# Kernel optimization log

Hardware: AMD Instinct MI355X
Metric: run time of the kernel (lower is better)

## Reference

```python
import jax, jax.numpy as jnp
import numpy as np

INPUT_DIM = 64
RESERVOIR_DIM = 2048
OUTPUT_DIM = 64
SPECTRAL_RADIUS = 0.9
LEAK_RATE = 0.3
SPARSITY = 0.9
INPUT_SCALING = 1.0
NOISE_LEVEL = 0.01
T = 4096


def setup_inputs() -> dict:
    key = jax.random.key(0)
    k_u, k_n = jax.random.split(key)
    u = jax.random.normal(k_u, (T, INPUT_DIM), dtype=jnp.float32)
    noise = jax.random.normal(k_n, (T, RESERVOIR_DIM), dtype=jnp.float32)

    # Reservoir weights, built exactly like the torch __init__ (fixed, untrained).
    rng = np.random.default_rng(0)
    W_in = (rng.standard_normal((RESERVOIR_DIM, INPUT_DIM)) * INPUT_SCALING).astype(np.float32)
    W = (rng.uniform(0.0, 1.0, (RESERVOIR_DIM, RESERVOIR_DIM)) * 2.0 - 1.0).astype(np.float32)
    mask = rng.uniform(0.0, 1.0, (RESERVOIR_DIM, RESERVOIR_DIM)) > SPARSITY
    W = W * mask.astype(np.float32)
    sr = np.max(np.abs(np.linalg.eigvals(W)))  # spectral radius normalization
    W = (W * (SPECTRAL_RADIUS / sr)).astype(np.float32)

    # nn.Linear(reservoir_dim, output_dim) init: U(-1/sqrt(N), 1/sqrt(N))
    bound = 1.0 / np.sqrt(RESERVOIR_DIM)
    readout_w = rng.uniform(-bound, bound, (OUTPUT_DIM, RESERVOIR_DIM)).astype(np.float32)
    readout_b = rng.uniform(-bound, bound, (OUTPUT_DIM,)).astype(np.float32)

    return {
        "u": u,
        "noise": noise,
        "W_in": jnp.asarray(W_in),
        "W": jnp.asarray(W),
        "readout_w": jnp.asarray(readout_w),
        "readout_b": jnp.asarray(readout_b),
    }


def reference(u, noise, W_in, W, readout_w, readout_b):
    # Leaky-integrated ESN recurrence, state reset to zeros (reset_state=True).
    input_terms = u @ W_in.T + noise * NOISE_LEVEL  # [T, N], precompute input GEMM

    def step(state, it):
        new_state = jnp.tanh(it + W @ state)
        state = (1.0 - LEAK_RATE) * state + LEAK_RATE * new_state
        return state, state

    init = jnp.zeros((RESERVOIR_DIM,), dtype=u.dtype)
    _, states = jax.lax.scan(step, init, input_terms)  # states: [T, N]
    return states @ readout_w.T + readout_b  # [T, output_dim]
```

## Files before the change

### kernel.cpp

```cpp
#include <hip/hip_runtime.h>

#define T_STEPS 4096
#define N_RES   2048
#define N_IN    64
#define N_OUT   64
#define LEAK    0.3f
#define NOISE_S 0.01f

#define NWG      128
#define RPW      16
#define RPWAVE   4
#define NTHREADS 320

typedef unsigned int uint32x4 __attribute__((ext_vector_type(4)));

__global__ __launch_bounds__(256) void input_terms_kernel(
    const float* __restrict__ u, const float* __restrict__ noise,
    const float* __restrict__ W_in, float* __restrict__ it) {
  const int t = blockIdx.x;
  const int tid = threadIdx.x;
  __shared__ float su[N_IN];
  if (tid < N_IN) su[tid] = u[(size_t)t * N_IN + tid];
  __syncthreads();
  #pragma unroll
  for (int k = 0; k < N_RES / 256; ++k) {
    const int n = tid + 256 * k;
    const float4* wr = reinterpret_cast<const float4*>(W_in + (size_t)n * N_IN);
    float acc = 0.f;
    #pragma unroll
    for (int j = 0; j < N_IN / 4; ++j) {
      float4 w4 = wr[j];
      acc = fmaf(w4.x, su[4 * j + 0], acc);
      acc = fmaf(w4.y, su[4 * j + 1], acc);
      acc = fmaf(w4.z, su[4 * j + 2], acc);
      acc = fmaf(w4.w, su[4 * j + 3], acc);
    }
    it[(size_t)t * N_RES + n] = acc + NOISE_S * noise[(size_t)t * N_RES + n];
  }
}

__global__ __launch_bounds__(NTHREADS, 1) void reservoir_kernel(
    const float* __restrict__ W, float* __restrict__ it,
    unsigned int* sbuf) {
  const int wg = blockIdx.x;
  const int tid = threadIdx.x;
  const int wave = tid >> 6;
  const int lane = tid & 63;
  const int R = wg * RPW;

  __shared__ float Wl[RPW * N_RES];
  __shared__ float ls[2][N_RES];

  {
    const float4* Wg = reinterpret_cast<const float4*>(W + (size_t)R * N_RES);
    float4* Wd = reinterpret_cast<float4*>(Wl);
    for (int idx = tid; idx < RPW * N_RES / 4; idx += NTHREADS)
      Wd[idx] = Wg[idx];
  }
  for (int idx = tid; idx < N_RES; idx += NTHREADS) ls[0][idx] = 0.f;
  __syncthreads();

  if (wave < 4) {
    const int r0 = R + wave * RPWAVE;
    const float4* W0 = reinterpret_cast<const float4*>(Wl + (size_t)(RPWAVE * wave + 0) * N_RES);
    const float4* W1 = reinterpret_cast<const float4*>(Wl + (size_t)(RPWAVE * wave + 1) * N_RES);
    const float4* W2 = reinterpret_cast<const float4*>(Wl + (size_t)(RPWAVE * wave + 2) * N_RES);
    const float4* W3 = reinterpret_cast<const float4*>(Wl + (size_t)(RPWAVE * wave + 3) * N_RES);

    float itv = 0.f;
    if (lane < RPWAVE) itv = it[r0 + lane];

    for (unsigned int t = 0; t < T_STEPS; ++t) {
      const float* cur = ls[t & 1];
      float* nxt = ls[(t + 1) & 1];
      unsigned int* swb = sbuf + ((t + 1) & 1) * N_RES;

      const float4* S4 = reinterpret_cast<const float4*>(cur);
      float a0 = 0.f, a1 = 0.f, a2 = 0.f, a3 = 0.f;
      #pragma unroll
      for (int j = 0; j < N_RES / 4 / 64; ++j) {
        const float4 s4 = S4[lane + 64 * j];
        const float4 x0 = W0[lane + 64 * j];
        const float4 x1 = W1[lane + 64 * j];
        const float4 x2 = W2[lane + 64 * j];
        const float4 x3 = W3[lane + 64 * j];
        a0 = fmaf(x0.x, s4.x, a0); a0 = fmaf(x0.y, s4.y, a0);
        a0 = fmaf(x0.z, s4.z, a0); a0 = fmaf(x0.w, s4.w, a0);
        a1 = fmaf(x1.x, s4.x, a1); a1 = fmaf(x1.y, s4.y, a1);
        a1 = fmaf(x1.z, s4.z, a1); a1 = fmaf(x1.w, s4.w, a1);
        a2 = fmaf(x2.x, s4.x, a2); a2 = fmaf(x2.y, s4.y, a2);
        a2 = fmaf(x2.z, s4.z, a2); a2 = fmaf(x2.w, s4.w, a2);
        a3 = fmaf(x3.x, s4.x, a3); a3 = fmaf(x3.y, s4.y, a3);
        a3 = fmaf(x3.z, s4.z, a3); a3 = fmaf(x3.w, s4.w, a3);
      }
      #pragma unroll
      for (int off = 32; off > 0; off >>= 1) {
        a0 += __shfl_xor(a0, off);
        a1 += __shfl_xor(a1, off);
        a2 += __shfl_xor(a2, off);
        a3 += __shfl_xor(a3, off);
      }

      const unsigned int tg = (t + 1) & 3u;
      unsigned int pkw = 0;
      if (lane < RPWAVE) {
        const float a = (lane == 0) ? a0 : (lane == 1) ? a1 : (lane == 2) ? a2 : a3;
        const float h = tanhf(itv + a);
        const float sold = cur[r0 + lane];
        const float snew = (1.0f - LEAK) * sold + LEAK * h;
        pkw = (__float_as_uint(snew) & ~3u) | tg;
        nxt[r0 + lane] = __uint_as_float(pkw);
        it[(size_t)t * N_RES + r0 + lane] = snew;
      }
      uint32x4 pk;
      pk[0] = __shfl(pkw, 0);
      pk[1] = __shfl(pkw, 1);
      pk[2] = __shfl(pkw, 2);
      pk[3] = __shfl(pkw, 3);
      if (lane == 0) {
        uint32x4* dst = reinterpret_cast<uint32x4*>(swb) + (r0 >> 2);
        asm volatile("global_store_dwordx4 %0, %1, off sc0 sc1"
                     :: "v"(dst), "v"(pk) : "memory");
      }
      if (lane < RPWAVE && t + 1 < T_STEPS)
        itv = it[(size_t)(t + 1) * N_RES + r0 + lane];

      __syncthreads();
    }
  } else {
    unsigned int ownmask = 0;
    {
      const int j = lane - ((wg * 4) & 63);
      if (0 <= j && j < 4) ownmask = 1u << (wg >> 4);
    }
    for (unsigned int t = 0; t < T_STEPS; ++t) {
      if (t + 1 < T_STEPS) {
        unsigned int* swb = sbuf + ((t + 1) & 1) * N_RES;
        float* nxt = ls[(t + 1) & 1];
        const unsigned int tg = (t + 1) & 3u;
        const char* p0 = (const char*)swb + lane * 16;
        const char* p1 = p0 + 4096;
        uint32x4* dst = reinterpret_cast<uint32x4*>(nxt);
        unsigned int need = 0xFFu & ~ownmask;
        for (;;) {
          uint32x4 v0, v1, v2, v3, v4, v5, v6, v7;
          asm volatile(
              "global_load_dwordx4 %0, %8, off sc0 sc1\n\t"
              "global_load_dwordx4 %1, %8, off offset:1024 sc0 sc1\n\t"
              "global_load_dwordx4 %2, %8, off offset:2048 sc0 sc1\n\t"
              "global_load_dwordx4 %3, %8, off offset:3072 sc0 sc1\n\t"
              "global_load_dwordx4 %4, %9, off sc0 sc1\n\t"
              "global_load_dwordx4 %5, %9, off offset:1024 sc0 sc1\n\t"
              "global_load_dwordx4 %6, %9, off offset:2048 sc0 sc1\n\t"
              "global_load_dwordx4 %7, %9, off offset:3072 sc0 sc1\n\t"
              "s_waitcnt vmcnt(0)"
              : "=&v"(v0), "=&v"(v1), "=&v"(v2), "=&v"(v3),
                "=&v"(v4), "=&v"(v5), "=&v"(v6), "=&v"(v7)
              : "v"(p0), "v"(p1)
              : "memory");
          if ((need & 1u)   && ((((v0[0]^tg)|(v0[1]^tg)|(v0[2]^tg)|(v0[3]^tg))&3u)==0u)) { dst[lane +   0] = v0; need &= ~1u; }
          if ((need & 2u)   && ((((v1[0]^tg)|(v1[1]^tg)|(v1[2]^tg)|(v1[3]^tg))&3u)==0u)) { dst[lane +  64] = v1; need &= ~2u; }
          if ((need & 4u)   && ((((v2[0]^tg)|(v2[1]^tg)|(v2[2]^tg)|(v2[3]^tg))&3u)==0u)) { dst[lane + 128] = v2; need &= ~4u; }
          if ((need & 8u)   && ((((v3[0]^tg)|(v3[1]^tg)|(v3[2]^tg)|(v3[3]^tg))&3u)==0u)) { dst[lane + 192] = v3; need &= ~8u; }
          if ((need & 16u)  && ((((v4[0]^tg)|(v4[1]^tg)|(v4[2]^tg)|(v4[3]^tg))&3u)==0u)) { dst[lane + 256] = v4; need &= ~16u; }
          if ((need & 32u)  && ((((v5[0]^tg)|(v5[1]^tg)|(v5[2]^tg)|(v5[3]^tg))&3u)==0u)) { dst[lane + 320] = v5; need &= ~32u; }
          if ((need & 64u)  && ((((v6[0]^tg)|(v6[1]^tg)|(v6[2]^tg)|(v6[3]^tg))&3u)==0u)) { dst[lane + 384] = v6; need &= ~64u; }
          if ((need & 128u) && ((((v7[0]^tg)|(v7[1]^tg)|(v7[2]^tg)|(v7[3]^tg))&3u)==0u)) { dst[lane + 448] = v7; need &= ~128u; }
          if (__all(need == 0u)) break;
          __builtin_amdgcn_s_sleep(1);
        }
      }
      __syncthreads();
    }
  }
}

__global__ __launch_bounds__(256) void readout_kernel(
    const float* __restrict__ states, const float* __restrict__ rw,
    const float* __restrict__ rb, float* __restrict__ out) {
  const int t = blockIdx.x;
  const int tid = threadIdx.x;
  const int o = tid & 63;
  const int q = tid >> 6;
  __shared__ float ss[N_RES];
  #pragma unroll
  for (int k = 0; k < N_RES / 256; ++k)
    ss[tid + 256 * k] = states[(size_t)t * N_RES + tid + 256 * k];
  __syncthreads();

  const float4* r4 = reinterpret_cast<const float4*>(rw + (size_t)o * N_RES + q * 512);
  float acc = 0.f;
  #pragma unroll 8
  for (int j = 0; j < 128; ++j) {
    float4 w4 = r4[j];
    const int base = q * 512 + 4 * j;
    acc = fmaf(w4.x, ss[base + 0], acc);
    acc = fmaf(w4.y, ss[base + 1], acc);
    acc = fmaf(w4.z, ss[base + 2], acc);
    acc = fmaf(w4.w, ss[base + 3], acc);
  }
  __shared__ float red[256];
  red[tid] = acc;
  __syncthreads();
  if (tid < 64) {
    float v = red[tid] + red[tid + 64] + red[tid + 128] + red[tid + 192];
    out[(size_t)t * N_OUT + tid] = v + rb[tid];
  }
}

extern "C" void kernel_launch(void* const* d_in, const int* in_sizes, int n_in,
                              void* d_out, int out_size, void* d_ws, size_t ws_size,
                              hipStream_t stream) {
  const float* u     = (const float*)d_in[0];
  const float* noise = (const float*)d_in[1];
  const float* W_in  = (const float*)d_in[2];
  const float* W     = (const float*)d_in[3];
  const float* rw    = (const float*)d_in[4];
  const float* rb    = (const float*)d_in[5];
  float* out = (float*)d_out;

  float* it = (float*)d_ws;
  unsigned int* sbuf =
      (unsigned int*)((char*)d_ws + (size_t)T_STEPS * N_RES * sizeof(float));

  hipMemsetAsync(sbuf, 0, 2 * N_RES * sizeof(unsigned int), stream);

  input_terms_kernel<<<T_STEPS, 256, 0, stream>>>(u, noise, W_in, it);

  void* args[] = {(void*)&W, (void*)&it, (void*)&sbuf};
  hipLaunchCooperativeKernel((void*)reservoir_kernel, dim3(NWG), dim3(NTHREADS),
                             args, 0, stream);

  readout_kernel<<<T_STEPS, 256, 0, stream>>>(it, rw, rb, out);
}
```

Before: 13.11 ms.

## Keep W rows in registers and offload input-term I/O to a helper wave

Each compute wave now loads its four W rows straight into 32 float4 registers instead of staging them in LDS, which removes per-step LDS reads of weights. A sixth wave is added that prefetches the next step's input terms into a small LDS staging buffer and writes finished states back to global memory, taking those global accesses off the compute waves' critical path. This raises register pressure and adds a one-step lag on the state writeback, and the stored states now carry the two low tag bits.

```diff
diff --git a/kernel.cpp b/kernel.cpp
--- a/kernel.cpp
+++ b/kernel.cpp
@@ -10,9 +10,10 @@
 #define NWG      128
 #define RPW      16
 #define RPWAVE   4
-#define NTHREADS 320
+#define NTHREADS 384
 
 typedef unsigned int uint32x4 __attribute__((ext_vector_type(4)));
+typedef float        floatx4 __attribute__((ext_vector_type(4)));
 
 __global__ __launch_bounds__(256) void input_terms_kernel(
     const float* __restrict__ u, const float* __restrict__ noise,
@@ -48,42 +49,54 @@
   const int lane = tid & 63;
   const int R = wg * RPW;
 
-  __shared__ float Wl[RPW * N_RES];
   __shared__ float ls[2][N_RES];
-
-  {
-    const float4* Wg = reinterpret_cast<const float4*>(W + (size_t)R * N_RES);
-    float4* Wd = reinterpret_cast<float4*>(Wl);
-    for (int idx = tid; idx < RPW * N_RES / 4; idx += NTHREADS)
-      Wd[idx] = Wg[idx];
-  }
+  __shared__ float stg_it[2][RPW];
+
   for (int idx = tid; idx < N_RES; idx += NTHREADS) ls[0][idx] = 0.f;
-  __syncthreads();
+  if (wave == 5 && lane < RPW) stg_it[0][lane] = it[R + lane];
 
   if (wave < 4) {
     const int r0 = R + wave * RPWAVE;
-    const float4* W0 = reinterpret_cast<const float4*>(Wl + (size_t)(RPWAVE * wave + 0) * N_RES);
-    const float4* W1 = reinterpret_cast<const float4*>(Wl + (size_t)(RPWAVE * wave + 1) * N_RES);
-    const float4* W2 = reinterpret_cast<const float4*>(Wl + (size_t)(RPWAVE * wave + 2) * N_RES);
-    const float4* W3 = reinterpret_cast<const float4*>(Wl + (size_t)(RPWAVE * wave + 3) * N_RES);
-
-    float itv = 0.f;
-    if (lane < RPWAVE) itv = it[r0 + lane];
+
+    floatx4 w[32];
+    #pragma unroll
+    for (int r = 0; r < RPWAVE; ++r) {
+      const char* p0 = (const char*)(W + (size_t)(r0 + r) * N_RES) + lane * 16;
+      const char* p1 = p0 + 4096;
+      asm volatile(
+          "global_load_dwordx4 %0, %8, off\n\t"
+          "global_load_dwordx4 %1, %8, off offset:1024\n\t"
+          "global_load_dwordx4 %2, %8, off offset:2048\n\t"
+          "global_load_dwordx4 %3, %8, off offset:3072\n\t"
+          "global_load_dwordx4 %4, %9, off\n\t"
+          "global_load_dwordx4 %5, %9, off offset:1024\n\t"
+          "global_load_dwordx4 %6, %9, off offset:2048\n\t"
+          "global_load_dwordx4 %7, %9, off offset:3072"
+          : "=&v"(w[8 * r + 0]), "=&v"(w[8 * r + 1]),
+            "=&v"(w[8 * r + 2]), "=&v"(w[8 * r + 3]),
+            "=&v"(w[8 * r + 4]), "=&v"(w[8 * r + 5]),
+            "=&v"(w[8 * r + 6]), "=&v"(w[8 * r + 7])
+          : "v"(p0), "v"(p1)
+          : "memory");
+    }
+    asm volatile("s_waitcnt vmcnt(0)" ::: "memory");
+    __builtin_amdgcn_sched_barrier(0);
+    __syncthreads();
 
     for (unsigned int t = 0; t < T_STEPS; ++t) {
       const float* cur = ls[t & 1];
       float* nxt = ls[(t + 1) & 1];
       unsigned int* swb = sbuf + ((t + 1) & 1) * N_RES;
 
-      const float4* S4 = reinterpret_cast<const float4*>(cur);
+      const floatx4* S4 = reinterpret_cast<const floatx4*>(cur);
       float a0 = 0.f, a1 = 0.f, a2 = 0.f, a3 = 0.f;
       #pragma unroll
-      for (int j = 0; j < N_RES / 4 / 64; ++j) {
-        const float4 s4 = S4[lane + 64 * j];
-        const float4 x0 = W0[lane + 64 * j];
-        const float4 x1 = W1[lane + 64 * j];
-        const float4 x2 = W2[lane + 64 * j];
-        const float4 x3 = W3[lane + 64 * j];
+      for (int j = 0; j < 8; ++j) {
+        const floatx4 s4 = S4[lane + 64 * j];
+        const floatx4 x0 = w[j];
+        const floatx4 x1 = w[8 + j];
+        const floatx4 x2 = w[16 + j];
+        const floatx4 x3 = w[24 + j];
         a0 = fmaf(x0.x, s4.x, a0); a0 = fmaf(x0.y, s4.y, a0);
         a0 = fmaf(x0.z, s4.z, a0); a0 = fmaf(x0.w, s4.w, a0);
         a1 = fmaf(x1.x, s4.x, a1); a1 = fmaf(x1.y, s4.y, a1);
@@ -105,12 +118,12 @@
       unsigned int pkw = 0;
       if (lane < RPWAVE) {
         const float a = (lane == 0) ? a0 : (lane == 1) ? a1 : (lane == 2) ? a2 : a3;
+        const float itv = stg_it[t & 1][wave * RPWAVE + lane];
         const float h = tanhf(itv + a);
         const float sold = cur[r0 + lane];
         const float snew = (1.0f - LEAK) * sold + LEAK * h;
         pkw = (__float_as_uint(snew) & ~3u) | tg;
         nxt[r0 + lane] = __uint_as_float(pkw);
-        it[(size_t)t * N_RES + r0 + lane] = snew;
       }
       uint32x4 pk;
       pk[0] = __shfl(pkw, 0);
@@ -122,12 +135,10 @@
         asm volatile("global_store_dwordx4 %0, %1, off sc0 sc1"
                      :: "v"(dst), "v"(pk) : "memory");
       }
-      if (lane < RPWAVE && t + 1 < T_STEPS)
-        itv = it[(size_t)(t + 1) * N_RES + r0 + lane];
-
       __syncthreads();
     }
-  } else {
+  } else if (wave == 4) {
+    __syncthreads();
     unsigned int ownmask = 0;
     {
       const int j = lane - ((wg * 4) & 63);
@@ -172,6 +183,19 @@
       }
       __syncthreads();
     }
+  } else {
+    __syncthreads();
+    for (unsigned int t = 0; t < T_STEPS; ++t) {
+      if (lane < RPW) {
+        if (t >= 1)
+          it[(size_t)(t - 1) * N_RES + R + lane] = ls[t & 1][R + lane];
+        if (t + 1 < T_STEPS)
+          stg_it[(t + 1) & 1][lane] = it[(size_t)(t + 1) * N_RES + R + lane];
+      }
+      __syncthreads();
+    }
+    if (lane < RPW)
+      it[(size_t)(T_STEPS - 1) * N_RES + R + lane] = ls[T_STEPS & 1][R + lane];
   }
 }
 
```

New measurement: 14.23 ms. 8.5% more time.

## Spread reservoir rows over 256 workgroups and offload input and state I/O to a dedicated wave

Applied to the files above, without the earlier changes.

Halves the rows per workgroup, from 16 to 8, and doubles the workgroup count to 256, so each compute wave does a 2-row dot product per step instead of 4. The per-row flag granularity in the shared exchange buffer becomes 8-byte halves, with matching dwordx2 publish stores and poll checks. A new seventh wave prefetches the next step's input term into LDS and writes the previous state back to global memory, taking that latency off the compute waves. In exchange, twice as many workgroups must meet at the cross-workgroup barrier each step. The two poller waves also duplicate the same polling work, and the stored states carry the 2-bit tag in their low mantissa bits.

```diff
diff --git a/kernel.cpp b/kernel.cpp
--- a/kernel.cpp
+++ b/kernel.cpp
@@ -7,12 +7,13 @@
 #define LEAK    0.3f
 #define NOISE_S 0.01f
 
-#define NWG      128
-#define RPW      16
-#define RPWAVE   4
-#define NTHREADS 320
+#define NWG      256
+#define RPW      8
+#define RPWAVE   2
+#define NTHREADS 448
 
 typedef unsigned int uint32x4 __attribute__((ext_vector_type(4)));
+typedef unsigned int uint32x2 __attribute__((ext_vector_type(2)));
 
 __global__ __launch_bounds__(256) void input_terms_kernel(
     const float* __restrict__ u, const float* __restrict__ noise,
@@ -50,6 +51,7 @@
 
   __shared__ float Wl[RPW * N_RES];
   __shared__ float ls[2][N_RES];
+  __shared__ float stg_it[2][RPW];
 
   {
     const float4* Wg = reinterpret_cast<const float4*>(W + (size_t)R * N_RES);
@@ -58,17 +60,13 @@
       Wd[idx] = Wg[idx];
   }
   for (int idx = tid; idx < N_RES; idx += NTHREADS) ls[0][idx] = 0.f;
+  if (wave == 6 && lane < RPW) stg_it[0][lane] = it[R + lane];
   __syncthreads();
 
   if (wave < 4) {
     const int r0 = R + wave * RPWAVE;
     const float4* W0 = reinterpret_cast<const float4*>(Wl + (size_t)(RPWAVE * wave + 0) * N_RES);
     const float4* W1 = reinterpret_cast<const float4*>(Wl + (size_t)(RPWAVE * wave + 1) * N_RES);
-    const float4* W2 = reinterpret_cast<const float4*>(Wl + (size_t)(RPWAVE * wave + 2) * N_RES);
-    const float4* W3 = reinterpret_cast<const float4*>(Wl + (size_t)(RPWAVE * wave + 3) * N_RES);
-
-    float itv = 0.f;
-    if (lane < RPWAVE) itv = it[r0 + lane];
 
     for (unsigned int t = 0; t < T_STEPS; ++t) {
       const float* cur = ls[t & 1];
@@ -76,72 +74,59 @@
       unsigned int* swb = sbuf + ((t + 1) & 1) * N_RES;
 
       const float4* S4 = reinterpret_cast<const float4*>(cur);
-      float a0 = 0.f, a1 = 0.f, a2 = 0.f, a3 = 0.f;
+      float a0 = 0.f, a1 = 0.f;
       #pragma unroll
-      for (int j = 0; j < N_RES / 4 / 64; ++j) {
+      for (int j = 0; j < 8; ++j) {
         const float4 s4 = S4[lane + 64 * j];
         const float4 x0 = W0[lane + 64 * j];
         const float4 x1 = W1[lane + 64 * j];
-        const float4 x2 = W2[lane + 64 * j];
-        const float4 x3 = W3[lane + 64 * j];
         a0 = fmaf(x0.x, s4.x, a0); a0 = fmaf(x0.y, s4.y, a0);
         a0 = fmaf(x0.z, s4.z, a0); a0 = fmaf(x0.w, s4.w, a0);
         a1 = fmaf(x1.x, s4.x, a1); a1 = fmaf(x1.y, s4.y, a1);
         a1 = fmaf(x1.z, s4.z, a1); a1 = fmaf(x1.w, s4.w, a1);
-        a2 = fmaf(x2.x, s4.x, a2); a2 = fmaf(x2.y, s4.y, a2);
-        a2 = fmaf(x2.z, s4.z, a2); a2 = fmaf(x2.w, s4.w, a2);
-        a3 = fmaf(x3.x, s4.x, a3); a3 = fmaf(x3.y, s4.y, a3);
-        a3 = fmaf(x3.z, s4.z, a3); a3 = fmaf(x3.w, s4.w, a3);
       }
       #pragma unroll
       for (int off = 32; off > 0; off >>= 1) {
         a0 += __shfl_xor(a0, off);
         a1 += __shfl_xor(a1, off);
-        a2 += __shfl_xor(a2, off);
-        a3 += __shfl_xor(a3, off);
       }
 
       const unsigned int tg = (t + 1) & 3u;
       unsigned int pkw = 0;
       if (lane < RPWAVE) {
-        const float a = (lane == 0) ? a0 : (lane == 1) ? a1 : (lane == 2) ? a2 : a3;
+        const float a = lane ? a1 : a0;
+        const float itv = stg_it[t & 1][wave * RPWAVE + lane];
         const float h = tanhf(itv + a);
         const float sold = cur[r0 + lane];
         const float snew = (1.0f - LEAK) * sold + LEAK * h;
         pkw = (__float_as_uint(snew) & ~3u) | tg;
         nxt[r0 + lane] = __uint_as_float(pkw);
-        it[(size_t)t * N_RES + r0 + lane] = snew;
-      }
-      uint32x4 pk;
+      }
+      uint32x2 pk;
       pk[0] = __shfl(pkw, 0);
       pk[1] = __shfl(pkw, 1);
-      pk[2] = __shfl(pkw, 2);
-      pk[3] = __shfl(pkw, 3);
       if (lane == 0) {
-        uint32x4* dst = reinterpret_cast<uint32x4*>(swb) + (r0 >> 2);
-        asm volatile("global_store_dwordx4 %0, %1, off sc0 sc1"
+        uint32x2* dst = reinterpret_cast<uint32x2*>(swb + r0);
+        asm volatile("global_store_dwordx2 %0, %1, off sc0 sc1"
                      :: "v"(dst), "v"(pk) : "memory");
       }
-      if (lane < RPWAVE && t + 1 < T_STEPS)
-        itv = it[(size_t)(t + 1) * N_RES + r0 + lane];
-
       __syncthreads();
     }
-  } else {
-    unsigned int ownmask = 0;
-    {
-      const int j = lane - ((wg * 4) & 63);
-      if (0 <= j && j < 4) ownmask = 1u << (wg >> 4);
+  } else if (wave < 6) {
+    unsigned int own = 0;
+    #pragma unroll
+    for (int cc = 0; cc < 2; ++cc) {
+      const int c = 2 * wg + cc;
+      if ((c & 63) == lane) own |= 3u << (2 * (c >> 6));
     }
     for (unsigned int t = 0; t < T_STEPS; ++t) {
       if (t + 1 < T_STEPS) {
         unsigned int* swb = sbuf + ((t + 1) & 1) * N_RES;
-        float* nxt = ls[(t + 1) & 1];
+        uint32x2* dst2 = reinterpret_cast<uint32x2*>(ls[(t + 1) & 1]);
         const unsigned int tg = (t + 1) & 3u;
         const char* p0 = (const char*)swb + lane * 16;
         const char* p1 = p0 + 4096;
-        uint32x4* dst = reinterpret_cast<uint32x4*>(nxt);
-        unsigned int need = 0xFFu & ~ownmask;
+        unsigned int need = 0xFFFFu & ~own;
         for (;;) {
           uint32x4 v0, v1, v2, v3, v4, v5, v6, v7;
           asm volatile(
@@ -158,20 +143,40 @@
                 "=&v"(v4), "=&v"(v5), "=&v"(v6), "=&v"(v7)
               : "v"(p0), "v"(p1)
               : "memory");
-          if ((need & 1u)   && ((((v0[0]^tg)|(v0[1]^tg)|(v0[2]^tg)|(v0[3]^tg))&3u)==0u)) { dst[lane +   0] = v0; need &= ~1u; }
-          if ((need & 2u)   && ((((v1[0]^tg)|(v1[1]^tg)|(v1[2]^tg)|(v1[3]^tg))&3u)==0u)) { dst[lane +  64] = v1; need &= ~2u; }
-          if ((need & 4u)   && ((((v2[0]^tg)|(v2[1]^tg)|(v2[2]^tg)|(v2[3]^tg))&3u)==0u)) { dst[lane + 128] = v2; need &= ~4u; }
-          if ((need & 8u)   && ((((v3[0]^tg)|(v3[1]^tg)|(v3[2]^tg)|(v3[3]^tg))&3u)==0u)) { dst[lane + 192] = v3; need &= ~8u; }
-          if ((need & 16u)  && ((((v4[0]^tg)|(v4[1]^tg)|(v4[2]^tg)|(v4[3]^tg))&3u)==0u)) { dst[lane + 256] = v4; need &= ~16u; }
-          if ((need & 32u)  && ((((v5[0]^tg)|(v5[1]^tg)|(v5[2]^tg)|(v5[3]^tg))&3u)==0u)) { dst[lane + 320] = v5; need &= ~32u; }
-          if ((need & 64u)  && ((((v6[0]^tg)|(v6[1]^tg)|(v6[2]^tg)|(v6[3]^tg))&3u)==0u)) { dst[lane + 384] = v6; need &= ~64u; }
-          if ((need & 128u) && ((((v7[0]^tg)|(v7[1]^tg)|(v7[2]^tg)|(v7[3]^tg))&3u)==0u)) { dst[lane + 448] = v7; need &= ~128u; }
+          #define CHK_CHUNK(vk, k)                                            \
+            do {                                                              \
+              const unsigned int blo = 1u << (2 * (k));                       \
+              const unsigned int bhi = 2u << (2 * (k));                       \
+              if ((need & blo) && ((((vk[0] ^ tg) | (vk[1] ^ tg)) & 3u) == 0u)) { \
+                uint32x2 h_; h_[0] = vk[0]; h_[1] = vk[1];                    \
+                dst2[2 * (lane + 64 * (k))] = h_; need &= ~blo;               \
+              }                                                               \
+              if ((need & bhi) && ((((vk[2] ^ tg) | (vk[3] ^ tg)) & 3u) == 0u)) { \
+                uint32x2 h_; h_[0] = vk[2]; h_[1] = vk[3];                    \
+                dst2[2 * (lane + 64 * (k)) + 1] = h_; need &= ~bhi;           \
+              }                                                               \
+            } while (0)
+          CHK_CHUNK(v0, 0); CHK_CHUNK(v1, 1); CHK_CHUNK(v2, 2); CHK_CHUNK(v3, 3);
+          CHK_CHUNK(v4, 4); CHK_CHUNK(v5, 5); CHK_CHUNK(v6, 6); CHK_CHUNK(v7, 7);
+          #undef CHK_CHUNK
           if (__all(need == 0u)) break;
           __builtin_amdgcn_s_sleep(1);
         }
       }
       __syncthreads();
     }
+  } else {
+    for (unsigned int t = 0; t < T_STEPS; ++t) {
+      if (lane < RPW) {
+        if (t >= 1)
+          it[(size_t)(t - 1) * N_RES + R + lane] = ls[t & 1][R + lane];
+        if (t + 1 < T_STEPS)
+          stg_it[(t + 1) & 1][lane] = it[(size_t)(t + 1) * N_RES + R + lane];
+      }
+      __syncthreads();
+    }
+    if (lane < RPW)
+      it[(size_t)(T_STEPS - 1) * N_RES + R + lane] = ls[T_STEPS & 1][R + lane];
   }
 }
 
```

After: 16.50 ms. 25.8% more time.
